# Kernel tuning notes

Measured on AMD Instinct MI355X. Metric: run time of the kernel, lower is better.

The kernel has to match this reference:

```python
import jax, jax.numpy as jnp
import numpy as np

N, D, H, L, E, OUT, G = 2048, 128, 8, 8, 65536, 64, 16
HD = D // H            # head_dim = 16
SCALE = HD ** -0.5
EPS = 1e-5             # BatchNorm1d eps


def _batchnorm(x, gamma, beta):
    # training-mode BatchNorm1d: biased batch stats over the node axis
    m = jnp.mean(x, axis=0)
    v = jnp.var(x, axis=0)
    return gamma * (x - m) * jax.lax.rsqrt(v + EPS) + beta


def _forward(X, pos_enc, proj_W, proj_b, pe_W, pe_b,
             Wq, bq, Wk, bk, Wv, bv, Wo, bo,
             g1, beta1, W1, b1, W2, b2, g2, beta2,
             mlp_W1, mlp_b1, mlp_W2, mlp_b2,
             edge_index, graph_ids, num_graphs):
    n = X.shape[0]
    # dense adjacency; sparse_coo_tensor sums duplicate edges -> scatter-add
    A = jnp.zeros((n, n), jnp.float32).at[edge_index[0], edge_index[1]].add(1.0)
    h = X @ proj_W + proj_b + pos_enc @ pe_W + pe_b          # [N, D]
    for l in range(L):
        h1 = h
        # NOTE: faithful to torch: [N,D] row-major reshaped to [H,N,HD]
        q = (h @ Wq[l] + bq[l]).reshape(H, n, HD) * SCALE
        k = (h @ Wk[l] + bk[l]).reshape(H, n, HD)
        v = (h @ Wv[l] + bv[l]).reshape(H, n, HD)
        t = jnp.einsum('hnd,hmd->hnm', q, k)                 # [H,N,N]
        attn = jax.nn.softmax(t * A, axis=2)                 # multiply-mask, softmax over all N
        o = jnp.einsum('hnm,hmd->hnd', attn, v).reshape(n, D)
        h = _batchnorm(o @ Wo[l] + bo[l] + h1, g1[l], beta1[l])
        h2 = h
        h = jax.nn.relu(h @ W1[l] + b1[l]) @ W2[l] + b2[l]
        h = _batchnorm(h2 + h, g2[l], beta2[l])
    # SumNode: per-graph node sum
    pooled = jax.ops.segment_sum(h, graph_ids, num_segments=num_graphs)  # [G, D]
    return jax.nn.relu(pooled @ mlp_W1 + mlp_b1) @ mlp_W2 + mlp_b2       # [G, OUT]


def setup_inputs() -> dict:
    key = jax.random.key(0)
    ks = jax.random.split(key, 32)
    f = jnp.float32
    s = D ** -0.5
    inp = {
        'X': jax.random.normal(ks[0], (N, 4), f),
        'pos_enc': jax.random.normal(ks[1], (N, 2), f),
        'edge_index': jax.random.randint(ks[2], (2, E), 0, N),
        'graph_ids': jnp.sort(jax.random.randint(ks[3], (N,), 0, G)).astype(jnp.int32),
        'num_graphs': G,
        'proj_W': jax.random.normal(ks[4], (4, D), f) * 0.5,
        'proj_b': jnp.zeros((D,), f),
        'pe_W': jax.random.normal(ks[5], (2, D), f) * 0.5,
        'pe_b': jnp.zeros((D,), f),
        'Wq': jax.random.normal(ks[6], (L, D, D), f) * s,
        'bq': jnp.zeros((L, D), f),
        'Wk': jax.random.normal(ks[7], (L, D, D), f) * s,
        'bk': jnp.zeros((L, D), f),
        'Wv': jax.random.normal(ks[8], (L, D, D), f) * s,
        'bv': jnp.zeros((L, D), f),
        'Wo': jax.random.normal(ks[9], (L, D, D), f) * s,
        'bo': jnp.zeros((L, D), f),
        'g1': jnp.ones((L, D), f),
        'beta1': jnp.zeros((L, D), f),
        'W1': jax.random.normal(ks[10], (L, D, 2 * D), f) * s,
        'b1': jnp.zeros((L, 2 * D), f),
        'W2': jax.random.normal(ks[11], (L, 2 * D, D), f) * (2 * D) ** -0.5,
        'b2': jnp.zeros((L, D), f),
        'g2': jnp.ones((L, D), f),
        'beta2': jnp.zeros((L, D), f),
        'mlp_W1': jax.random.normal(ks[12], (D, D), f) * s,
        'mlp_b1': jnp.zeros((D,), f),
        'mlp_W2': jax.random.normal(ks[13], (D, OUT), f) * s,
        'mlp_b2': jnp.zeros((OUT,), f),
    }
    return inp


def reference(X, pos_enc, edge_index, graph_ids, num_graphs,
              proj_W, proj_b, pe_W, pe_b,
              Wq, bq, Wk, bk, Wv, bv, Wo, bo,
              g1, beta1, W1, b1, W2, b2, g2, beta2,
              mlp_W1, mlp_b1, mlp_W2, mlp_b2):
    return _forward(X, pos_enc, proj_W, proj_b, pe_W, pe_b,
                    Wq, bq, Wk, bk, Wv, bv, Wo, bo,
                    g1, beta1, W1, b1, W2, b2, g2, beta2,
                    mlp_W1, mlp_b1, mlp_W2, mlp_b2,
                    edge_index, graph_ids, num_graphs)
```

## Files before the change

kernel.cpp:

```cpp
#include <hip/hip_runtime.h>
#include <hip/hip_bf16.h>

#define NN 2048
#define DD 128
#define HH 8
#define HDIM 16
#define LL 8
#define GG 16
#define BNEPS 1e-5f

typedef unsigned int u32;
typedef unsigned long long u64;
typedef __attribute__((ext_vector_type(8))) short bf16x8;
typedef __attribute__((ext_vector_type(8))) unsigned short us8;
typedef __attribute__((ext_vector_type(4))) float f32x4;

__device__ __forceinline__ unsigned short f2bf(float f) {
    union { float f; u32 u; } v; v.f = f;
    u32 u = v.u;
    u32 r = (u + 0x7fffu + ((u >> 16) & 1u)) >> 16;
    return (unsigned short)r;
}

__global__ __launch_bounds__(256) void zero_k(uint4* __restrict__ p) {
    p[blockIdx.x * 256 + threadIdx.x] = make_uint4(0u, 0u, 0u, 0u);
}

__global__ __launch_bounds__(256) void scatter_k(const int* __restrict__ ei, u32* __restrict__ A, int E) {
    int e = blockIdx.x * 256 + threadIdx.x;
    if (e < E) {
        int s = ei[e];
        int d = ei[E + e];
        atomicAdd(&A[s * NN + d], 1u);
    }
}

__global__ __launch_bounds__(256) void count_k(const u32* __restrict__ A, u32* __restrict__ deg) {
    int r = blockIdx.x, t = threadIdx.x;
    __shared__ u32 sb[256];
    u32 c = 0;
    for (int j = t; j < NN; j += 256) c += (A[r * NN + j] != 0u) ? 1u : 0u;
    sb[t] = c; __syncthreads();
    for (int off = 128; off; off >>= 1) { if (t < off) sb[t] += sb[t + off]; __syncthreads(); }
    if (t == 0) deg[r] = sb[0];
}

__global__ __launch_bounds__(256) void scan_k(const u32* __restrict__ deg, u32* __restrict__ rowptr) {
    __shared__ u32 part[256];
    int t = threadIdx.x;
    u32 loc[8]; u32 s = 0;
#pragma unroll
    for (int i = 0; i < 8; i++) { loc[i] = deg[t * 8 + i]; s += loc[i]; }
    part[t] = s; __syncthreads();
    for (int off = 1; off < 256; off <<= 1) {
        u32 vprev = (t >= off) ? part[t - off] : 0u;
        __syncthreads();
        part[t] += vprev;
        __syncthreads();
    }
    u32 run = (t == 0) ? 0u : part[t - 1];
    if (t == 0) rowptr[0] = 0u;
#pragma unroll
    for (int i = 0; i < 8; i++) { run += loc[i]; rowptr[t * 8 + i + 1] = run; }
}

__global__ __launch_bounds__(256) void emit_k(const u32* __restrict__ A, const u32* __restrict__ rowptr,
                                              u32* __restrict__ colidx, u32* __restrict__ cntv) {
    int r = blockIdx.x, tid = threadIdx.x;
    int lane = tid & 63, wid = tid >> 6;
    __shared__ u32 wsum[4];
    u32 base = rowptr[r];
    u32 cb = 0;
    for (int c0 = 0; c0 < NN; c0 += 256) {
        int c = c0 + tid;
        u32 a = A[r * NN + c];
        bool p = (a != 0u);
        u64 bal = __ballot(p);
        u32 rankw = (u32)__popcll(bal & ((1ull << lane) - 1ull));
        if (lane == 0) wsum[wid] = (u32)__popcll(bal);
        __syncthreads();
        u32 woff = 0;
#pragma unroll
        for (int w2 = 0; w2 < 4; w2++) if (w2 < wid) woff += wsum[w2];
        u32 tot = wsum[0] + wsum[1] + wsum[2] + wsum[3];
        if (p) { u32 pos = base + cb + woff + rankw; colidx[pos] = (u32)c; cntv[pos] = a; }
        cb += tot;
        __syncthreads();
    }
}

__global__ __launch_bounds__(256) void wconv_k(const float* __restrict__ Wq, const float* __restrict__ Wk,
                                               const float* __restrict__ Wv, const float* __restrict__ Wo,
                                               const float* __restrict__ W1, const float* __restrict__ W2,
                                               us8* __restrict__ Wf) {
    int tid = blockIdx.x * 256 + threadIdx.x;
    int layer = tid >> 14;
    int r = tid & 16383;
// ... 21 lines not shown
    int col = nt * 16 + (lane & 15);
    int k0 = kt * 32 + (lane >> 4) * 8;
    us8 o;
#pragma unroll
    for (int j = 0; j < 8; j++) o[j] = f2bf(src[(k0 + j) * ld + col]);
    Wf[tid] = o;
}

__global__ __launch_bounds__(256) void h0_k(const float* __restrict__ X, const float* __restrict__ pe,
                                            const float* __restrict__ pW, const float* __restrict__ pb,
                                            const float* __restrict__ peW, const float* __restrict__ peb,
                                            float* __restrict__ h) {
    int idx = blockIdx.x * 256 + threadIdx.x;
    int r = idx >> 7, d = idx & 127;
    float acc = pb[d] + peb[d];
    acc += X[r * 4 + 0] * pW[0 * DD + d];
    acc += X[r * 4 + 1] * pW[1 * DD + d];
    acc += X[r * 4 + 2] * pW[2 * DD + d];
    acc += X[r * 4 + 3] * pW[3 * DD + d];
    acc += pe[r * 2 + 0] * peW[0 * DD + d];
    acc += pe[r * 2 + 1] * peW[1 * DD + d];
    h[idx] = acc;
}

__device__ __forceinline__ void finalize_stats2(const float* __restrict__ ps, const float* __restrict__ pss,
                                                const float* __restrict__ gamma, const float* __restrict__ beta,
                                                float* aS, float* cS, float* sred, int tidx) {
    if (ps) {
        int d = tidx & 127, half = tidx >> 7;
        float s = 0.f, s2 = 0.f;
        const float* p0 = ps + half * 64 * 128 + d;
        const float* p1 = pss + half * 64 * 128 + d;
#pragma unroll 8
        for (int i = 0; i < 64; i++) { s += p0[i * 128]; s2 += p1[i * 128]; }
        sred[tidx] = s;
        sred[256 + tidx] = s2;
        __syncthreads();
        if (tidx < 128) {
            float st = sred[tidx] + sred[tidx + 128];
            float s2t = sred[256 + tidx] + sred[256 + tidx + 128];
            float mean = st * (1.0f / NN);
            float var = s2t * (1.0f / NN) - mean * mean;
            float rstd = rsqrtf(var + BNEPS);
            float a = gamma[tidx] * rstd;
            aS[tidx] = a;
            cS[tidx] = beta[tidx] - mean * a;
        }
    } else if (tidx < 128) {
        aS[tidx] = 1.f;
        cS[tidx] = 0.f;
    }
}

__global__ __launch_bounds__(256) void qkv_k(const float* __restrict__ t,
                                             const float* __restrict__ ps, const float* __restrict__ pss,
                                             const float* __restrict__ gamma, const float* __restrict__ beta,
                                             const bf16x8* __restrict__ Wfl,
                                             const float* __restrict__ bq, const float* __restrict__ bk,
                                             const float* __restrict__ bv,
                                             float* __restrict__ q, float* __restrict__ k, float* __restrict__ v,
                                             float* __restrict__ psv) {
    __shared__ float aS[128], cS[128], sred[512];
    int tidx = threadIdx.x;
    finalize_stats2(ps, pss, gamma, beta, aS, cS, sred, tidx);
    __syncthreads();
    int strip = blockIdx.x;
    int m0 = strip * 16;
    int lane = tidx & 63, wv = tidx >> 6;
    int arow = m0 + (lane & 15);
    int k0b = (lane >> 4) * 8;
    bf16x8 af[4];
#pragma unroll
    for (int kt = 0; kt < 4; kt++) {
        int k0 = kt * 32 + k0b;
        const float* tp = t + arow * DD + k0;
        float4 v0 = *(const float4*)(tp);
        float4 v1 = *(const float4*)(tp + 4);
        float vals[8] = {v0.x, v0.y, v0.z, v0.w, v1.x, v1.y, v1.z, v1.w};
        bf16x8 f;
#pragma unroll
        for (int j = 0; j < 8; j++) f[j] = (short)f2bf(vals[j] * aS[k0 + j] + cS[k0 + j]);
        af[kt] = f;
    }
#pragma unroll
    for (int ti = 0; ti < 6; ti++) {
        int tile = wv * 6 + ti;
        int mat = tile >> 3, nt = tile & 7;
        const bf16x8* wb = Wfl + mat * 2048;
        f32x4 acc = {0.f, 0.f, 0.f, 0.f};
#pragma unroll
        for (int kt = 0; kt < 4; kt++)
            acc = __builtin_amdgcn_mfma_f32_16x16x32_bf16(af[kt], wb[(kt * 8 + nt) * 64 + lane], acc, 0, 0, 0);
        const float* bias = (mat == 0) ? bq : ((mat == 1) ? bk : bv);
        float* outp = (mat == 0) ? q : ((mat == 1) ? k : v);
        float scale = (mat == 0) ? 0.25f : 1.0f;
        int col = nt * 16 + (lane & 15);
        int r0 = m0 + (lane >> 4) * 4;
        float bb = bias[col];
        float vals[4];
#pragma unroll
        for (int j = 0; j < 4; j++) {
            vals[j] = (acc[j] + bb) * scale;
            outp[(r0 + j) * DD + col] = vals[j];
        }
        if (mat == 2) {
            float cs = vals[0] + vals[1] + vals[2] + vals[3];
            cs += __shfl_xor(cs, 16);
            cs += __shfl_xor(cs, 32);
            if (lane < 16) psv[strip * 128 + col] = cs;
        }
    }
}

__global__ __launch_bounds__(256) void attn2_k(const float* __restrict__ q, const float* __restrict__ kb,
                                               const float* __restrict__ vb, const u32* __restrict__ rowptr,
                                               const u32* __restrict__ colidx, const u32* __restrict__ cntv,
                                               const float* __restrict__ psv, unsigned short* __restrict__ obb) {
    int tid = threadIdx.x;
    int bid = blockIdx.x;
    int hh = bid >> 7;
    __shared__ float vred[16][17];
    __shared__ float vsS[16];
    {
        int d = tid & 15, part = tid >> 4;
        int strip = hh * 16 + part;
        float s = 0.f;
#pragma unroll
        for (int i = 0; i < 8; i++) s += psv[strip * 128 + i * 16 + d];
        vred[d][part] = s;
    }
    __syncthreads();
    if (tid < 16) {
        float s = 0.f;
#pragma unroll
        for (int i = 0; i < 16; i++) s += vred[tid][i];
        vsS[tid] = s;
    }
    __syncthreads();

    int lane = tid & 15;
    int gidx = bid * 16 + (tid >> 4);
    int nn = gidx & (NN - 1);
    const float* qr = q + hh * (NN * HDIM) + nn * HDIM;
    float qv[16];
    *(float4*)&qv[0]  = *(const float4*)(qr + 0);
    *(float4*)&qv[4]  = *(const float4*)(qr + 4);
    *(float4*)&qv[8]  = *(const float4*)(qr + 8);
    *(float4*)&qv[12] = *(const float4*)(qr + 12);
    int rs = (int)rowptr[nn], re = (int)rowptr[nn + 1];
    int deg = re - rs;

    float s[8];
    int mc[8];
    float lm = -1e30f;
#pragma unroll
    for (int ch = 0; ch < 8; ch++) {
        s[ch] = -1e30f; mc[ch] = 0;
        if (ch * 16 < deg) {
            int e = rs + ch * 16 + lane;
            if (e < re) {
                mc[ch] = (int)colidx[e];
                float c = (float)cntv[e];
                const float* kr = kb + hh * (NN * HDIM) + mc[ch] * HDIM;
                float kv[16];
                *(float4*)&kv[0]  = *(const float4*)(kr + 0);
                *(float4*)&kv[4]  = *(const float4*)(kr + 4);
                *(float4*)&kv[8]  = *(const float4*)(kr + 8);
                *(float4*)&kv[12] = *(const float4*)(kr + 12);
                float d = 0.f;
#pragma unroll
                for (int i = 0; i < 16; i++) d += qv[i] * kv[i];
                s[ch] = c * d;
            }
            lm = fmaxf(lm, s[ch]);
        }
// ... 14 lines not shown
    for (int off = 1; off < 16; off <<= 1) lm = fmaxf(lm, __shfl_xor(lm, off));
    float rowmax = fmaxf(lm, 0.f);
    float em = __expf(-rowmax);

    float z = 0.f;
    float acc[16];
#pragma unroll
    for (int i = 0; i < 16; i++) acc[i] = 0.f;
#pragma unroll
    for (int ch = 0; ch < 8; ch++) {
        if (ch * 16 < deg) {
            int e = rs + ch * 16 + lane;
            if (e < re) {
                float w = __expf(s[ch] - rowmax);
                z += w;
                float coef = w - em;
                const float* vr = vb + hh * (NN * HDIM) + mc[ch] * HDIM;
                float vv[16];
                *(float4*)&vv[0]  = *(const float4*)(vr + 0);
                *(float4*)&vv[4]  = *(const float4*)(vr + 4);
                *(float4*)&vv[8]  = *(const float4*)(vr + 8);
                *(float4*)&vv[12] = *(const float4*)(vr + 12);
#pragma unroll
                for (int i = 0; i < 16; i++) acc[i] += coef * vv[i];
            }
        }
    }
    for (int base = rs + 128; base < re; base += 16) {
        int e = base + lane;
        if (e < re) {
            int m2 = (int)colidx[e];
            float c = (float)cntv[e];
            const float* kr = kb + hh * (NN * HDIM) + m2 * HDIM;
            float d = 0.f;
#pragma unroll
            for (int i = 0; i < 16; i++) d += qv[i] * kr[i];
            float w = __expf(c * d - rowmax);
            z += w;
            float coef = w - em;
            const float* vr = vb + hh * (NN * HDIM) + m2 * HDIM;
#pragma unroll
            for (int i = 0; i < 16; i++) acc[i] += coef * vr[i];
        }
    }
#pragma unroll
    for (int off = 1; off < 16; off <<= 1) {
        z += __shfl_xor(z, off);
#pragma unroll
        for (int i = 0; i < 16; i++) acc[i] += __shfl_xor(acc[i], off);
    }
    if (lane == 0) {
        float Z = z + (float)(NN - deg) * em;
        float inv = 1.f / Z;
        unsigned short* orow = obb + hh * (NN * HDIM) + nn * HDIM;
        us8 lo, hi;
#pragma unroll
        for (int i = 0; i < 8; i++) {
            lo[i] = f2bf((acc[i] + em * vsS[i]) * inv);
            hi[i] = f2bf((acc[i + 8] + em * vsS[i + 8]) * inv);
        }
        *(us8*)(orow + 0) = lo;
        *(us8*)(orow + 8) = hi;
    }
}

__global__ __launch_bounds__(256) void gemmO_k(const unsigned short* __restrict__ obb,
                                               const bf16x8* __restrict__ Wfo,
                                               const float* __restrict__ bo,
                                               const float* __restrict__ tprev,
                                               const float* __restrict__ ps, const float* __restrict__ pss,
                                               const float* __restrict__ gamma, const float* __restrict__ beta,
                                               float* __restrict__ t1,
                                               float* __restrict__ ps1, float* __restrict__ pss1) {
    __shared__ float aS[128], cS[128], sred[512];
    int tidx = threadIdx.x;
    finalize_stats2(ps, pss, gamma, beta, aS, cS, sred, tidx);
    __syncthreads();
    int strip = blockIdx.x;
    int m0 = strip * 16;
    int lane = tidx & 63, wv = tidx >> 6;
    int arow = m0 + (lane & 15);
    int k0b = (lane >> 4) * 8;
    bf16x8 af[4];
#pragma unroll
    for (int kt = 0; kt < 4; kt++)
        af[kt] = *(const bf16x8*)(obb + arow * DD + kt * 32 + k0b);
#pragma unroll
    for (int ti = 0; ti < 2; ti++) {
        int nt = wv * 2 + ti;
        f32x4 acc = {0.f, 0.f, 0.f, 0.f};
#pragma unroll
        for (int kt = 0; kt < 4; kt++)
            acc = __builtin_amdgcn_mfma_f32_16x16x32_bf16(af[kt], Wfo[(kt * 8 + nt) * 64 + lane], acc, 0, 0, 0);
        int col = nt * 16 + (lane & 15);
        int r0 = m0 + (lane >> 4) * 4;
        float bb = bo[col];
        float a = aS[col], c = cS[col];
        float sum = 0.f, sumsq = 0.f;
#pragma unroll
        for (int j = 0; j < 4; j++) {
            float res = tprev[(r0 + j) * DD + col] * a + c;
            float v0 = acc[j] + bb + res;
            t1[(r0 + j) * DD + col] = v0;
            sum += v0; sumsq += v0 * v0;
        }
        sum += __shfl_xor(sum, 16);  sum += __shfl_xor(sum, 32);
        sumsq += __shfl_xor(sumsq, 16); sumsq += __shfl_xor(sumsq, 32);
        if (lane < 16) { ps1[strip * 128 + col] = sum; pss1[strip * 128 + col] = sumsq; }
    }
}

__global__ __launch_bounds__(256) void mlp_k(const float* __restrict__ t1,
                                             const float* __restrict__ ps1, const float* __restrict__ pss1,
                                             const float* __restrict__ g1, const float* __restrict__ be1,
                                             const bf16x8* __restrict__ Wf1, const float* __restrict__ b1,
                                             const bf16x8* __restrict__ Wf2, const float* __restrict__ b2,
                                             float* __restrict__ t2,
                                             float* __restrict__ ps2, float* __restrict__ pss2) {
    __shared__ float aS[128], cS[128], sred[512];
    __shared__ unsigned short midL[16][264];
    int tidx = threadIdx.x;
    finalize_stats2(ps1, pss1, g1, be1, aS, cS, sred, tidx);
    __syncthreads();
    int strip = blockIdx.x;
    int m0 = strip * 16;
    int lane = tidx & 63, wv = tidx >> 6;
    int lrow = lane & 15;
    int arow = m0 + lrow;
    int k0b = (lane >> 4) * 8;
    bf16x8 af[4];
#pragma unroll
    for (int kt = 0; kt < 4; kt++) {
        int k0 = kt * 32 + k0b;
        const float* tp = t1 + arow * DD + k0;
        float4 v0 = *(const float4*)(tp);
        float4 v1 = *(const float4*)(tp + 4);
        float vals[8] = {v0.x, v0.y, v0.z, v0.w, v1.x, v1.y, v1.z, v1.w};
        bf16x8 f;
#pragma unroll
        for (int j = 0; j < 8; j++) f[j] = (short)f2bf(vals[j] * aS[k0 + j] + cS[k0 + j]);
        af[kt] = f;
    }
#pragma unroll
    for (int ti = 0; ti < 4; ti++) {
        int nt = wv * 4 + ti;
        f32x4 acc = {0.f, 0.f, 0.f, 0.f};
#pragma unroll
        for (int kt = 0; kt < 4; kt++)
            acc = __builtin_amdgcn_mfma_f32_16x16x32_bf16(af[kt], Wf1[(kt * 16 + nt) * 64 + lane], acc, 0, 0, 0);
        int col = nt * 16 + (lane & 15);
        int r0l = (lane >> 4) * 4;
        float bb = b1[col];
#pragma unroll
        for (int j = 0; j < 4; j++)
            midL[r0l + j][col] = f2bf(fmaxf(acc[j] + bb, 0.f));
    }
    __syncthreads();
    bf16x8 af2[8];
#pragma unroll
    for (int kt = 0; kt < 8; kt++)
        af2[kt] = *(const bf16x8*)(&midL[lrow][kt * 32 + k0b]);
#pragma unroll
    for (int ti = 0; ti < 2; ti++) {
        int nt = wv * 2 + ti;
        f32x4 acc = {0.f, 0.f, 0.f, 0.f};
#pragma unroll
        for (int kt = 0; kt < 8; kt++)
            acc = __builtin_amdgcn_mfma_f32_16x16x32_bf16(af2[kt], Wf2[(kt * 8 + nt) * 64 + lane], acc, 0, 0, 0);
        int col = nt * 16 + (lane & 15);
        int r0 = m0 + (lane >> 4) * 4;
        float bb = b2[col];
        float a = aS[col], c = cS[col];
        float sum = 0.f, sumsq = 0.f;
#pragma unroll
        for (int j = 0; j < 4; j++) {
            float res = t1[(r0 + j) * DD + col] * a + c;
            float v0 = acc[j] + bb + res;
            t2[(r0 + j) * DD + col] = v0;
            sum += v0; sumsq += v0 * v0;
        }
        sum += __shfl_xor(sum, 16);  sum += __shfl_xor(sum, 32);
        sumsq += __shfl_xor(sumsq, 16); sumsq += __shfl_xor(sumsq, 32);
        if (lane < 16) { ps2[strip * 128 + col] = sum; pss2[strip * 128 + col] = sumsq; }
    }
}

__global__ __launch_bounds__(128) void poolpart_k(const float* __restrict__ t, const float* __restrict__ ps,
                                                  const float* __restrict__ pss, const float* __restrict__ gamma,
                                                  const float* __restrict__ beta, const int* __restrict__ gid,
                                                  float* __restrict__ poolp) {
    int g = blockIdx.x;
    int ch = blockIdx.y;
    int d = threadIdx.x;
    float s = 0.f, s2 = 0.f;
#pragma unroll 8
    for (int i = 0; i < 128; i++) { s += ps[i * 128 + d]; s2 += pss[i * 128 + d]; }
    float mean = s * (1.0f / NN);
    float var = s2 * (1.0f / NN) - mean * mean;
    float rstd = rsqrtf(var + BNEPS);
    float a = gamma[d] * rstd;
    float c = beta[d] - mean * a;
    int lo = 0, hi = NN;
    while (lo < hi) { int mid = (lo + hi) >> 1; if (gid[mid] < g) lo = mid + 1; else hi = mid; }
    int start = lo;
    lo = start; hi = NN;
    while (lo < hi) { int mid = (lo + hi) >> 1; if (gid[mid] <= g) lo = mid + 1; else hi = mid; }
    int end = lo;
    float acc = 0.f;
    for (int r = start + ch; r < end; r += 8) acc += t[r * DD + d] * a + c;
    poolp[(g * 8 + ch) * DD + d] = acc;
}

__global__ __launch_bounds__(256) void head_k(const float* __restrict__ poolp, const float* __restrict__ W1,
                                              const float* __restrict__ b1, const float* __restrict__ W2,
                                              const float* __restrict__ b2, float* __restrict__ out) {
    int g = blockIdx.x;
    __shared__ float p[128], midv[128];
    if (threadIdx.x < 128) {
        float s = 0.f;
#pragma unroll
        for (int c = 0; c < 8; c++) s += poolp[(g * 8 + c) * DD + threadIdx.x];
        p[threadIdx.x] = s;
    }
    __syncthreads();
    if (threadIdx.x < 128) {
        int d = threadIdx.x;
        float acc = b1[d];
        for (int k2 = 0; k2 < 128; k2++) acc += p[k2] * W1[k2 * 128 + d];
        midv[d] = fmaxf(acc, 0.f);
    }
    __syncthreads();
    if (threadIdx.x < 64) {
        int j = threadIdx.x;
        float acc = b2[j];
        for (int k2 = 0; k2 < 128; k2++) acc += midv[k2] * W2[k2 * 64 + j];
        out[g * 64 + j] = acc;
    }
}

extern "C" void kernel_launch(void* const* d_in, const int* in_sizes, int n_in,
                              void* d_out, int out_size, void* d_ws, size_t ws_size,
                              hipStream_t stream) {
    (void)n_in; (void)out_size; (void)ws_size;
    const float* X      = (const float*)d_in[0];
    const float* pos    = (const float*)d_in[1];
    const int*   ei     = (const int*)d_in[2];
    const int*   gid    = (const int*)d_in[3];
    const float* proj_W = (const float*)d_in[5];
    const float* proj_b = (const float*)d_in[6];
    const float* pe_W   = (const float*)d_in[7];
    const float* pe_b   = (const float*)d_in[8];
    const float* Wq     = (const float*)d_in[9];
    const float* bq     = (const float*)d_in[10];
    const float* Wk     = (const float*)d_in[11];
    const float* bk     = (const float*)d_in[12];
    const float* Wv     = (const float*)d_in[13];
    const float* bv     = (const float*)d_in[14];
    const float* Wo     = (const float*)d_in[15];
    const float* bo     = (const float*)d_in[16];
    const float* g1     = (const float*)d_in[17];
    const float* beta1  = (const float*)d_in[18];
    const float* W1     = (const float*)d_in[19];
    const float* b1     = (const float*)d_in[20];
    const float* W2     = (const float*)d_in[21];
    const float* b2     = (const float*)d_in[22];
    const float* g2     = (const float*)d_in[23];
    const float* beta2  = (const float*)d_in[24];
    const float* mW1    = (const float*)d_in[25];
    const float* mb1    = (const float*)d_in[26];
    const float* mW2    = (const float*)d_in[27];
    const float* mb2    = (const float*)d_in[28];
    float* out = (float*)d_out;

    int E = in_sizes[2] / 2;

    char* w = (char*)d_ws;
    u32*   Adense = (u32*)(w + 0);
    u32*   deg    = (u32*)(w + 16777216);
    u32*   rowptr = (u32*)(w + 16785408);
    u32*   colidx = (u32*)(w + 16793856);
    u32*   cntv   = (u32*)(w + 17056000);
    float* tA     = (float*)(w + 17318144);
    float* tB     = (float*)(w + 18366720);
    float* qb     = (float*)(w + 19415296);
    float* kb     = (float*)(w + 20463872);
    float* vb     = (float*)(w + 21512448);
    unsigned short* obb = (unsigned short*)(w + 22561024);
    float* psA    = (float*)(w + 23085312);
    float* pssA   = (float*)(w + 23150848);
    float* psB    = (float*)(w + 23216384);
    float* pssB   = (float*)(w + 23281920);
    float* psv    = (float*)(w + 23347456);
    bf16x8* Wf    = (bf16x8*)(w + 23421184);
    float* poolp  = (float*)(w + 25518336);

    zero_k<<<4096, 256, 0, stream>>>((uint4*)Adense);
    scatter_k<<<(E + 255) / 256, 256, 0, stream>>>(ei, Adense, E);
    count_k<<<NN, 256, 0, stream>>>(Adense, deg);
    scan_k<<<1, 256, 0, stream>>>(deg, rowptr);
    emit_k<<<NN, 256, 0, stream>>>(Adense, rowptr, colidx, cntv);

    wconv_k<<<512, 256, 0, stream>>>(Wq, Wk, Wv, Wo, W1, W2, (us8*)Wf);

    h0_k<<<NN * DD / 256, 256, 0, stream>>>(X, pos, proj_W, proj_b, pe_W, pe_b, tA);

    for (int l = 0; l < LL; l++) {
        const bf16x8* Wfl = Wf + l * 16384;
        const float* psIn  = (l == 0) ? nullptr : psA;
        const float* pssIn = (l == 0) ? nullptr : pssA;
        const float* gIn   = (l == 0) ? nullptr : (g2 + (l - 1) * DD);
        const float* bIn   = (l == 0) ? nullptr : (beta2 + (l - 1) * DD);

        qkv_k<<<128, 256, 0, stream>>>(tA, psIn, pssIn, gIn, bIn, Wfl,
                                       bq + l * DD, bk + l * DD, bv + l * DD, qb, kb, vb, psv);
        attn2_k<<<HH * NN / 16, 256, 0, stream>>>(qb, kb, vb, rowptr, colidx, cntv, psv, obb);
        gemmO_k<<<128, 256, 0, stream>>>(obb, Wfl + 6144, bo + l * DD, tA, psIn, pssIn, gIn, bIn,
                                         tB, psB, pssB);
        mlp_k<<<128, 256, 0, stream>>>(tB, psB, pssB, g1 + l * DD, beta1 + l * DD,
                                       Wfl + 8192, b1 + l * 2 * DD, Wfl + 12288, b2 + l * DD,
                                       tA, psA, pssA);
    }

    poolpart_k<<<dim3(GG, 8), 128, 0, stream>>>(tA, psA, pssA, g2 + 7 * DD, beta2 + 7 * DD, gid, poolp);
    head_k<<<GG, 256, 0, stream>>>(poolp, mW1, mb1, mW2, mb2, out);
}
```

Baseline: 336.7 us.

## Fuse per-layer kernels into one persistent cooperative kernel with grid syncs

After: 431.8 us. 1.28x slower.

```diff
diff --git a/kernel.cpp b/kernel.cpp
--- a/kernel.cpp
+++ b/kernel.cpp
@@ -1,4 +1,5 @@
 #include <hip/hip_runtime.h>
+#include <hip/hip_cooperative_groups.h>
 #include <hip/hip_bf16.h>
 
 #define NN 2048
@@ -8,6 +9,8 @@
 #define LL 8
 #define GG 16
 #define BNEPS 1e-5f
+
+namespace cg = cooperative_groups;
 
 typedef unsigned int u32;
 typedef unsigned long long u64;
@@ -170,19 +173,17 @@
     }
 }
 
-__global__ __launch_bounds__(256) void qkv_k(const float* __restrict__ t,
-                                             const float* __restrict__ ps, const float* __restrict__ pss,
-                                             const float* __restrict__ gamma, const float* __restrict__ beta,
-                                             const bf16x8* __restrict__ Wfl,
-                                             const float* __restrict__ bq, const float* __restrict__ bk,
-                                             const float* __restrict__ bv,
-                                             float* __restrict__ q, float* __restrict__ k, float* __restrict__ v,
-                                             float* __restrict__ psv) {
+__device__ void qkv_phase(const float* __restrict__ t,
+                          const float* __restrict__ ps, const float* __restrict__ pss,
+                          const float* __restrict__ gamma, const float* __restrict__ beta,
+                          const bf16x8* __restrict__ Wfl,
+                          const float* __restrict__ bq, const float* __restrict__ bk,
+                          const float* __restrict__ bv,
+                          float* __restrict__ q, float* __restrict__ k, float* __restrict__ v,
+                          float* __restrict__ psv, int strip, int tidx) {
     __shared__ float aS[128], cS[128], sred[512];
-    int tidx = threadIdx.x;
     finalize_stats2(ps, pss, gamma, beta, aS, cS, sred, tidx);
     __syncthreads();
-    int strip = blockIdx.x;
     int m0 = strip * 16;
     int lane = tidx & 63, wv = tidx >> 6;
     int arow = m0 + (lane & 15);
@@ -230,12 +231,11 @@
     }
 }
 
-__global__ __launch_bounds__(256) void attn2_k(const float* __restrict__ q, const float* __restrict__ kb,
-                                               const float* __restrict__ vb, const u32* __restrict__ rowptr,
-                                               const u32* __restrict__ colidx, const u32* __restrict__ cntv,
-                                               const float* __restrict__ psv, unsigned short* __restrict__ obb) {
-    int tid = threadIdx.x;
-    int bid = blockIdx.x;
+__device__ void attn_phase(const float* __restrict__ q, const float* __restrict__ kb,
+                           const float* __restrict__ vb, const u32* __restrict__ rowptr,
+                           const u32* __restrict__ colidx, const u32* __restrict__ cntv,
+                           const float* __restrict__ psv, unsigned short* __restrict__ obb,
+                           int bid, int tid) {
     int hh = bid >> 7;
     __shared__ float vred[16][17];
     __shared__ float vsS[16];
@@ -371,19 +371,17 @@
     }
 }
 
-__global__ __launch_bounds__(256) void gemmO_k(const unsigned short* __restrict__ obb,
-                                               const bf16x8* __restrict__ Wfo,
-                                               const float* __restrict__ bo,
-                                               const float* __restrict__ tprev,
-                                               const float* __restrict__ ps, const float* __restrict__ pss,
-                                               const float* __restrict__ gamma, const float* __restrict__ beta,
-                                               float* __restrict__ t1,
-                                               float* __restrict__ ps1, float* __restrict__ pss1) {
+__device__ void gemmO_phase(const unsigned short* __restrict__ obb,
+                            const bf16x8* __restrict__ Wfo,
+                            const float* __restrict__ bo,
+                            const float* __restrict__ tprev,
+                            const float* __restrict__ ps, const float* __restrict__ pss,
+                            const float* __restrict__ gamma, const float* __restrict__ beta,
+                            float* __restrict__ t1,
+                            float* __restrict__ ps1, float* __restrict__ pss1, int strip, int tidx) {
     __shared__ float aS[128], cS[128], sred[512];
-    int tidx = threadIdx.x;
     finalize_stats2(ps, pss, gamma, beta, aS, cS, sred, tidx);
     __syncthreads();
-    int strip = blockIdx.x;
     int m0 = strip * 16;
     int lane = tidx & 63, wv = tidx >> 6;
     int arow = m0 + (lane & 15);
@@ -417,19 +415,17 @@
     }
 }
 
-__global__ __launch_bounds__(256) void mlp_k(const float* __restrict__ t1,
-                                             const float* __restrict__ ps1, const float* __restrict__ pss1,
-                                             const float* __restrict__ g1, const float* __restrict__ be1,
-                                             const bf16x8* __restrict__ Wf1, const float* __restrict__ b1,
-                                             const bf16x8* __restrict__ Wf2, const float* __restrict__ b2,
-                                             float* __restrict__ t2,
-                                             float* __restrict__ ps2, float* __restrict__ pss2) {
+__device__ void mlp_phase(const float* __restrict__ t1,
+                          const float* __restrict__ ps1, const float* __restrict__ pss1,
+                          const float* __restrict__ g1, const float* __restrict__ be1,
+                          const bf16x8* __restrict__ Wf1, const float* __restrict__ b1,
+                          const bf16x8* __restrict__ Wf2, const float* __restrict__ b2,
+                          float* __restrict__ t2,
+                          float* __restrict__ ps2, float* __restrict__ pss2, int strip, int tidx) {
     __shared__ float aS[128], cS[128], sred[512];
     __shared__ unsigned short midL[16][264];
-    int tidx = threadIdx.x;
     finalize_stats2(ps1, pss1, g1, be1, aS, cS, sred, tidx);
     __syncthreads();
-    int strip = blockIdx.x;
     int m0 = strip * 16;
     int lane = tidx & 63, wv = tidx >> 6;
     int lrow = lane & 15;
@@ -492,13 +488,14 @@
     }
 }
 
-__global__ __launch_bounds__(128) void poolpart_k(const float* __restrict__ t, const float* __restrict__ ps,
-                                                  const float* __restrict__ pss, const float* __restrict__ gamma,
-                                                  const float* __restrict__ beta, const int* __restrict__ gid,
-                                                  float* __restrict__ poolp) {
-    int g = blockIdx.x;
-    int ch = blockIdx.y;
-    int d = threadIdx.x;
+__device__ void poolpart_phase(const float* __restrict__ t, const float* __restrict__ ps,
+                               const float* __restrict__ pss, const float* __restrict__ gamma,
+                               const float* __restrict__ beta, const int* __restrict__ gid,
+                               float* __restrict__ poolp, int bid, int tidx) {
+    if (tidx >= 128) return;
+    int g = bid >> 3;
+    int ch = bid & 7;
+    int d = tidx;
     float s = 0.f, s2 = 0.f;
 #pragma unroll 8
     for (int i = 0; i < 128; i++) { s += ps[i * 128 + d]; s2 += pss[i * 128 + d]; }
@@ -518,31 +515,109 @@
     poolp[(g * 8 + ch) * DD + d] = acc;
 }
 
-__global__ __launch_bounds__(256) void head_k(const float* __restrict__ poolp, const float* __restrict__ W1,
-                                              const float* __restrict__ b1, const float* __restrict__ W2,
-                                              const float* __restrict__ b2, float* __restrict__ out) {
-    int g = blockIdx.x;
+__device__ void head_phase(const float* __restrict__ poolp, const float* __restrict__ W1,
+                           const float* __restrict__ b1, const float* __restrict__ W2,
+                           const float* __restrict__ b2, float* __restrict__ out, int g, int tidx) {
     __shared__ float p[128], midv[128];
-    if (threadIdx.x < 128) {
+    if (tidx < 128) {
         float s = 0.f;
 #pragma unroll
-        for (int c = 0; c < 8; c++) s += poolp[(g * 8 + c) * DD + threadIdx.x];
-        p[threadIdx.x] = s;
+        for (int c = 0; c < 8; c++) s += poolp[(g * 8 + c) * DD + tidx];
+        p[tidx] = s;
     }
     __syncthreads();
-    if (threadIdx.x < 128) {
-        int d = threadIdx.x;
+    if (tidx < 128) {
+        int d = tidx;
         float acc = b1[d];
         for (int k2 = 0; k2 < 128; k2++) acc += p[k2] * W1[k2 * 128 + d];
         midv[d] = fmaxf(acc, 0.f);
     }
     __syncthreads();
-    if (threadIdx.x < 64) {
-        int j = threadIdx.x;
+    if (tidx < 64) {
+        int j = tidx;
         float acc = b2[j];
         for (int k2 = 0; k2 < 128; k2++) acc += midv[k2] * W2[k2 * 64 + j];
         out[g * 64 + j] = acc;
     }
+}
+
+struct LayerParams {
+    const u32 *rowptr, *colidx, *cntv;
+    const bf16x8* Wf;
+    const float *bq, *bk, *bv, *bo, *g1, *be1, *b1, *b2, *g2, *be2;
+    const float *mW1, *mb1, *mW2, *mb2;
+    const int* gid;
+    float *tA, *tB, *qb, *kb, *vb;
+    unsigned short* obb;
+    float *psA, *pssA, *psB, *pssB, *psv, *poolp;
+    float* out;
+};
+
+__global__ __launch_bounds__(256, 4) void layers_k(LayerParams P) {
+    cg::grid_group grid = cg::this_grid();
+    int bid = blockIdx.x, tidx = threadIdx.x;
+#pragma clang loop unroll(disable)
+    for (int l = 0; l < LL; l++) {
+        const bf16x8* Wfl = P.Wf + l * 16384;
+        const float* psIn  = (l == 0) ? nullptr : P.psA;
+        const float* pssIn = (l == 0) ? nullptr : P.pssA;
+        const float* gIn   = (l == 0) ? nullptr : (P.g2 + (l - 1) * DD);
+        const float* bIn   = (l == 0) ? nullptr : (P.be2 + (l - 1) * DD);
+        if (bid < 128)
+            qkv_phase(P.tA, psIn, pssIn, gIn, bIn, Wfl, P.bq + l * DD, P.bk + l * DD, P.bv + l * DD,
+                      P.qb, P.kb, P.vb, P.psv, bid, tidx);
+        grid.sync();
+        attn_phase(P.qb, P.kb, P.vb, P.rowptr, P.colidx, P.cntv, P.psv, P.obb, bid, tidx);
+        grid.sync();
+        if (bid < 128)
+            gemmO_phase(P.obb, Wfl + 6144, P.bo + l * DD, P.tA, psIn, pssIn, gIn, bIn,
+                        P.tB, P.psB, P.pssB, bid, tidx);
+        grid.sync();
+        if (bid < 128)
+            mlp_phase(P.tB, P.psB, P.pssB, P.g1 + l * DD, P.be1 + l * DD,
+                      Wfl + 8192, P.b1 + l * 2 * DD, Wfl + 12288, P.b2 + l * DD,
+                      P.tA, P.psA, P.pssA, bid, tidx);
+        grid.sync();
+    }
+    if (bid < 128)
+        poolpart_phase(P.tA, P.psA, P.pssA, P.g2 + 7 * DD, P.be2 + 7 * DD, P.gid, P.poolp, bid, tidx);
+    grid.sync();
+    if (bid < 16)
+        head_phase(P.poolp, P.mW1, P.mb1, P.mW2, P.mb2, P.out, bid, tidx);
+}
+
+__global__ __launch_bounds__(256) void qkv_k(const float* t, const float* ps, const float* pss,
+                                             const float* gamma, const float* beta, const bf16x8* Wfl,
+                                             const float* bq, const float* bk, const float* bv,
+                                             float* q, float* k, float* v, float* psv) {
+    qkv_phase(t, ps, pss, gamma, beta, Wfl, bq, bk, bv, q, k, v, psv, blockIdx.x, threadIdx.x);
+}
+__global__ __launch_bounds__(256) void attn2_k(const float* q, const float* kb, const float* vb,
+                                               const u32* rowptr, const u32* colidx, const u32* cntv,
+                                               const float* psv, unsigned short* obb) {
+    attn_phase(q, kb, vb, rowptr, colidx, cntv, psv, obb, blockIdx.x, threadIdx.x);
+}
+__global__ __launch_bounds__(256) void gemmO_k(const unsigned short* obb, const bf16x8* Wfo, const float* bo,
+                                               const float* tprev, const float* ps, const float* pss,
+                                               const float* gamma, const float* beta,
+                                               float* t1, float* ps1, float* pss1) {
+    gemmO_phase(obb, Wfo, bo, tprev, ps, pss, gamma, beta, t1, ps1, pss1, blockIdx.x, threadIdx.x);
+}
+__global__ __launch_bounds__(256) void mlp_k(const float* t1, const float* ps1, const float* pss1,
+                                             const float* g1, const float* be1,
+                                             const bf16x8* Wf1, const float* b1,
+                                             const bf16x8* Wf2, const float* b2,
+                                             float* t2, float* ps2, float* pss2) {
+    mlp_phase(t1, ps1, pss1, g1, be1, Wf1, b1, Wf2, b2, t2, ps2, pss2, blockIdx.x, threadIdx.x);
+}
+__global__ __launch_bounds__(256) void poolpart_k(const float* t, const float* ps, const float* pss,
+                                                  const float* gamma, const float* beta, const int* gid,
+                                                  float* poolp) {
+    poolpart_phase(t, ps, pss, gamma, beta, gid, poolp, blockIdx.x, threadIdx.x);
+}
+__global__ __launch_bounds__(256) void head_k(const float* poolp, const float* W1, const float* b1,
+                                              const float* W2, const float* b2, float* out) {
+    head_phase(poolp, W1, b1, W2, b2, out, blockIdx.x, threadIdx.x);
 }
 
 extern "C" void kernel_launch(void* const* d_in, const int* in_sizes, int n_in,
@@ -611,23 +686,46 @@
 
     h0_k<<<NN * DD / 256, 256, 0, stream>>>(X, pos, proj_W, proj_b, pe_W, pe_b, tA);
 
-    for (int l = 0; l < LL; l++) {
-        const bf16x8* Wfl = Wf + l * 16384;
-        const float* psIn  = (l == 0) ? nullptr : psA;
-        const float* pssIn = (l == 0) ? nullptr : pssA;
-        const float* gIn   = (l == 0) ? nullptr : (g2 + (l - 1) * DD);
-        const float* bIn   = (l == 0) ? nullptr : (beta2 + (l - 1) * DD);
-
-        qkv_k<<<128, 256, 0, stream>>>(tA, psIn, pssIn, gIn, bIn, Wfl,
-                                       bq + l * DD, bk + l * DD, bv + l * DD, qb, kb, vb, psv);
-        attn2_k<<<HH * NN / 16, 256, 0, stream>>>(qb, kb, vb, rowptr, colidx, cntv, psv, obb);
-        gemmO_k<<<128, 256, 0, stream>>>(obb, Wfl + 6144, bo + l * DD, tA, psIn, pssIn, gIn, bIn,
-                                         tB, psB, pssB);
-        mlp_k<<<128, 256, 0, stream>>>(tB, psB, pssB, g1 + l * DD, beta1 + l * DD,
-                                       Wfl + 8192, b1 + l * 2 * DD, Wfl + 12288, b2 + l * DD,
-                                       tA, psA, pssA);
-    }
-
-    poolpart_k<<<dim3(GG, 8), 128, 0, stream>>>(tA, psA, pssA, g2 + 7 * DD, beta2 + 7 * DD, gid, poolp);
-    head_k<<<GG, 256, 0, stream>>>(poolp, mW1, mb1, mW2, mb2, out);
-}
+    LayerParams hp;
+    hp.rowptr = rowptr; hp.colidx = colidx; hp.cntv = cntv;
+    hp.Wf = Wf;
+    hp.bq = bq; hp.bk = bk; hp.bv = bv; hp.bo = bo;
+    hp.g1 = g1; hp.be1 = beta1; hp.b1 = b1; hp.b2 = b2; hp.g2 = g2; hp.be2 = beta2;
+    hp.mW1 = mW1; hp.mb1 = mb1; hp.mW2 = mW2; hp.mb2 = mb2;
+    hp.gid = gid;
+    hp.tA = tA; hp.tB = tB; hp.qb = qb; hp.kb = kb; hp.vb = vb;
+    hp.obb = obb;
+    hp.psA = psA; hp.pssA = pssA; hp.psB = psB; hp.pssB = pssB; hp.psv = psv; hp.poolp = poolp;
+    hp.out = out;
+
+    bool coop_ok = false;
+    int nb = 0;
+    if (hipOccupancyMaxActiveBlocksPerMultiprocessor(&nb, (const void*)layers_k, 256, 0) == hipSuccess) {
+        if (nb >= 4) coop_ok = true;
+    }
+    hipError_t ce = hipErrorUnknown;
+    if (coop_ok) {
+        void* kargs[] = { (void*)&hp };
+        ce = hipLaunchCooperativeKernel((const void*)layers_k, dim3(1024), dim3(256), kargs, 0, stream);
+    }
+    if (ce != hipSuccess) {
+        (void)hipGetLastError();
+        for (int l = 0; l < LL; l++) {
+            const bf16x8* Wfl = Wf + l * 16384;
+            const float* psIn  = (l == 0) ? nullptr : psA;
+            const float* pssIn = (l == 0) ? nullptr : pssA;
+            const float* gIn   = (l == 0) ? nullptr : (g2 + (l - 1) * DD);
+            const float* bIn   = (l == 0) ? nullptr : (beta2 + (l - 1) * DD);
+            qkv_k<<<128, 256, 0, stream>>>(tA, psIn, pssIn, gIn, bIn, Wfl,
+                                           bq + l * DD, bk + l * DD, bv + l * DD, qb, kb, vb, psv);
+            attn2_k<<<HH * NN / 16, 256, 0, stream>>>(qb, kb, vb, rowptr, colidx, cntv, psv, obb);
+            gemmO_k<<<128, 256, 0, stream>>>(obb, Wfl + 6144, bo + l * DD, tA, psIn, pssIn, gIn, bIn,
+                                             tB, psB, pssB);
+            mlp_k<<<128, 256, 0, stream>>>(tB, psB, pssB, g1 + l * DD, beta1 + l * DD,
+                                           Wfl + 8192, b1 + l * 2 * DD, Wfl + 12288, b2 + l * DD,
+                                           tA, psA, pssA);
+        }
+        poolpart_k<<<128, 256, 0, stream>>>(tA, psA, pssA, g2 + 7 * DD, beta2 + 7 * DD, gid, poolp);
+        head_k<<<GG, 256, 0, stream>>>(poolp, mW1, mb1, mW2, mb2, out);
+    }
+}
```

## Fuse output projection into attention kernel and merge pooling with head MLP

Applied to the files above, without the earlier changes.

After: 473.1 us. 1.41x slower.

```diff
diff --git a/kernel.cpp b/kernel.cpp
--- a/kernel.cpp
+++ b/kernel.cpp
@@ -170,6 +170,30 @@
     }
 }
 
+__device__ __forceinline__ void finalize_stats_1024(const float* __restrict__ ps, const float* __restrict__ pss,
+                                                    const float* __restrict__ gamma, const float* __restrict__ beta,
+                                                    float* aS, float* cS, float* sred, int tidx) {
+    int d = tidx & 127, half = tidx >> 7;
+    float s = 0.f, s2 = 0.f;
+    const float* p0 = ps + half * 512 * 128 + d;
+    const float* p1 = pss + half * 512 * 128 + d;
+#pragma unroll 8
+    for (int i = 0; i < 512; i++) { s += p0[i * 128]; s2 += p1[i * 128]; }
+    sred[tidx] = s;
+    sred[256 + tidx] = s2;
+    __syncthreads();
+    if (tidx < 128) {
+        float st = sred[tidx] + sred[tidx + 128];
+        float s2t = sred[256 + tidx] + sred[256 + tidx + 128];
+        float mean = st * (1.0f / NN);
+        float var = s2t * (1.0f / NN) - mean * mean;
+        float rstd = rsqrtf(var + BNEPS);
+        float a = gamma[tidx] * rstd;
+        aS[tidx] = a;
+        cS[tidx] = beta[tidx] - mean * a;
+    }
+}
+
 __global__ __launch_bounds__(256) void qkv_k(const float* __restrict__ t,
                                              const float* __restrict__ ps, const float* __restrict__ pss,
                                              const float* __restrict__ gamma, const float* __restrict__ beta,
@@ -177,7 +201,7 @@
                                              const float* __restrict__ bq, const float* __restrict__ bk,
                                              const float* __restrict__ bv,
                                              float* __restrict__ q, float* __restrict__ k, float* __restrict__ v,
-                                             float* __restrict__ psv) {
+                                             float* __restrict__ psv, float* __restrict__ tnorm) {
     __shared__ float aS[128], cS[128], sred[512];
     int tidx = threadIdx.x;
     finalize_stats2(ps, pss, gamma, beta, aS, cS, sred, tidx);
@@ -195,9 +219,17 @@
         float4 v0 = *(const float4*)(tp);
         float4 v1 = *(const float4*)(tp + 4);
         float vals[8] = {v0.x, v0.y, v0.z, v0.w, v1.x, v1.y, v1.z, v1.w};
+        float vn[8];
         bf16x8 f;
 #pragma unroll
-        for (int j = 0; j < 8; j++) f[j] = (short)f2bf(vals[j] * aS[k0 + j] + cS[k0 + j]);
+        for (int j = 0; j < 8; j++) {
+            vn[j] = vals[j] * aS[k0 + j] + cS[k0 + j];
+            f[j] = (short)f2bf(vn[j]);
+        }
+        if (wv == 0) {
+            *(float4*)(tnorm + arow * DD + k0)     = make_float4(vn[0], vn[1], vn[2], vn[3]);
+            *(float4*)(tnorm + arow * DD + k0 + 4) = make_float4(vn[4], vn[5], vn[6], vn[7]);
+        }
         af[kt] = f;
     }
 #pragma unroll
@@ -233,12 +265,17 @@
 __global__ __launch_bounds__(256) void attn2_k(const float* __restrict__ q, const float* __restrict__ kb,
                                                const float* __restrict__ vb, const u32* __restrict__ rowptr,
                                                const u32* __restrict__ colidx, const u32* __restrict__ cntv,
-                                               const float* __restrict__ psv, unsigned short* __restrict__ obb) {
+                                               const float* __restrict__ psv,
+                                               const bf16x8* __restrict__ Wfo, const float* __restrict__ bo,
+                                               const float* __restrict__ tnorm,
+                                               float* __restrict__ t1,
+                                               float* __restrict__ psB, float* __restrict__ pssB) {
     int tid = threadIdx.x;
     int bid = blockIdx.x;
     int hh = bid >> 7;
     __shared__ float vred[16][17];
     __shared__ float vsS[16];
+    __shared__ unsigned short oL[16][16];
     {
         int d = tid & 15, part = tid >> 4;
         int strip = hh * 16 + part;
@@ -359,61 +396,45 @@
     if (lane == 0) {
         float Z = z + (float)(NN - deg) * em;
         float inv = 1.f / Z;
-        unsigned short* orow = obb + hh * (NN * HDIM) + nn * HDIM;
-        us8 lo, hi;
-#pragma unroll
-        for (int i = 0; i < 8; i++) {
-            lo[i] = f2bf((acc[i] + em * vsS[i]) * inv);
-            hi[i] = f2bf((acc[i + 8] + em * vsS[i + 8]) * inv);
-        }
-        *(us8*)(orow + 0) = lo;
-        *(us8*)(orow + 8) = hi;
-    }
-}
-
-__global__ __launch_bounds__(256) void gemmO_k(const unsigned short* __restrict__ obb,
-                                               const bf16x8* __restrict__ Wfo,
-                                               const float* __restrict__ bo,
-                                               const float* __restrict__ tprev,
-                                               const float* __restrict__ ps, const float* __restrict__ pss,
-                                               const float* __restrict__ gamma, const float* __restrict__ beta,
-                                               float* __restrict__ t1,
-                                               float* __restrict__ ps1, float* __restrict__ pss1) {
-    __shared__ float aS[128], cS[128], sred[512];
-    int tidx = threadIdx.x;
-    finalize_stats2(ps, pss, gamma, beta, aS, cS, sred, tidx);
-    __syncthreads();
-    int strip = blockIdx.x;
-    int m0 = strip * 16;
-    int lane = tidx & 63, wv = tidx >> 6;
-    int arow = m0 + (lane & 15);
-    int k0b = (lane >> 4) * 8;
+        int grp = tid >> 4;
+#pragma unroll
+        for (int i = 0; i < 16; i++) oL[grp][i] = f2bf((acc[i] + em * vsS[i]) * inv);
+    }
+    __syncthreads();
+
+    int l64 = tid & 63, w = tid >> 6;
+    int row = l64 & 15, kq = l64 >> 4;
     bf16x8 af[4];
-#pragma unroll
-    for (int kt = 0; kt < 4; kt++)
-        af[kt] = *(const bf16x8*)(obb + arow * DD + kt * 32 + k0b);
+    if (row < 2) {
+#pragma unroll
+        for (int kt = 0; kt < 4; kt++)
+            af[kt] = *(const bf16x8*)&oL[row * 8 + kt * 2 + (kq >> 1)][(kq & 1) * 8];
+    } else {
+        bf16x8 zf = {0, 0, 0, 0, 0, 0, 0, 0};
+#pragma unroll
+        for (int kt = 0; kt < 4; kt++) af[kt] = zf;
+    }
 #pragma unroll
     for (int ti = 0; ti < 2; ti++) {
-        int nt = wv * 2 + ti;
-        f32x4 acc = {0.f, 0.f, 0.f, 0.f};
+        int nt = w * 2 + ti;
+        f32x4 oacc = {0.f, 0.f, 0.f, 0.f};
 #pragma unroll
         for (int kt = 0; kt < 4; kt++)
-            acc = __builtin_amdgcn_mfma_f32_16x16x32_bf16(af[kt], Wfo[(kt * 8 + nt) * 64 + lane], acc, 0, 0, 0);
-        int col = nt * 16 + (lane & 15);
-        int r0 = m0 + (lane >> 4) * 4;
-        float bb = bo[col];
-        float a = aS[col], c = cS[col];
-        float sum = 0.f, sumsq = 0.f;
-#pragma unroll
-        for (int j = 0; j < 4; j++) {
-            float res = tprev[(r0 + j) * DD + col] * a + c;
-            float v0 = acc[j] + bb + res;
-            t1[(r0 + j) * DD + col] = v0;
-            sum += v0; sumsq += v0 * v0;
-        }
-        sum += __shfl_xor(sum, 16);  sum += __shfl_xor(sum, 32);
-        sumsq += __shfl_xor(sumsq, 16); sumsq += __shfl_xor(sumsq, 32);
-        if (lane < 16) { ps1[strip * 128 + col] = sum; pss1[strip * 128 + col] = sumsq; }
+            oacc = __builtin_amdgcn_mfma_f32_16x16x32_bf16(af[kt], Wfo[(kt * 8 + nt) * 64 + l64], oacc, 0, 0, 0);
+        if (kq == 0) {
+            int col = nt * 16 + row;
+            float bb = bo[col];
+            float sum = 0.f, sumsq = 0.f;
+#pragma unroll
+            for (int j = 0; j < 2; j++) {
+                int r = 2 * bid + j;
+                float v0 = oacc[j] + bb + tnorm[r * DD + col];
+                t1[r * DD + col] = v0;
+                sum += v0; sumsq += v0 * v0;
+            }
+            psB[bid * 128 + col] = sum;
+            pssB[bid * 128 + col] = sumsq;
+        }
     }
 }
 
@@ -427,7 +448,7 @@
     __shared__ float aS[128], cS[128], sred[512];
     __shared__ unsigned short midL[16][264];
     int tidx = threadIdx.x;
-    finalize_stats2(ps1, pss1, g1, be1, aS, cS, sred, tidx);
+    finalize_stats_1024(ps1, pss1, g1, be1, aS, cS, sred, tidx);
     __syncthreads();
     int strip = blockIdx.x;
     int m0 = strip * 16;
@@ -492,56 +513,41 @@
     }
 }
 
-__global__ __launch_bounds__(128) void poolpart_k(const float* __restrict__ t, const float* __restrict__ ps,
-                                                  const float* __restrict__ pss, const float* __restrict__ gamma,
-                                                  const float* __restrict__ beta, const int* __restrict__ gid,
-                                                  float* __restrict__ poolp) {
-    int g = blockIdx.x;
-    int ch = blockIdx.y;
-    int d = threadIdx.x;
-    float s = 0.f, s2 = 0.f;
-#pragma unroll 8
-    for (int i = 0; i < 128; i++) { s += ps[i * 128 + d]; s2 += pss[i * 128 + d]; }
-    float mean = s * (1.0f / NN);
-    float var = s2 * (1.0f / NN) - mean * mean;
-    float rstd = rsqrtf(var + BNEPS);
-    float a = gamma[d] * rstd;
-    float c = beta[d] - mean * a;
+__global__ __launch_bounds__(256) void pool_head_k(const float* __restrict__ t, const float* __restrict__ ps,
+                                                   const float* __restrict__ pss, const float* __restrict__ gamma,
+                                                   const float* __restrict__ beta, const int* __restrict__ gid,
+                                                   const float* __restrict__ W1, const float* __restrict__ b1,
+                                                   const float* __restrict__ W2, const float* __restrict__ b2,
+                                                   float* __restrict__ out) {
+    __shared__ float aS[128], cS[128], sred[512];
+    __shared__ float psum[2][128];
+    __shared__ float p[128], midv[128];
+    int tidx = threadIdx.x, g = blockIdx.x;
+    finalize_stats2(ps, pss, gamma, beta, aS, cS, sred, tidx);
+    __syncthreads();
     int lo = 0, hi = NN;
     while (lo < hi) { int mid = (lo + hi) >> 1; if (gid[mid] < g) lo = mid + 1; else hi = mid; }
     int start = lo;
     lo = start; hi = NN;
     while (lo < hi) { int mid = (lo + hi) >> 1; if (gid[mid] <= g) lo = mid + 1; else hi = mid; }
     int end = lo;
+    int d = tidx & 127, half = tidx >> 7;
     float acc = 0.f;
-    for (int r = start + ch; r < end; r += 8) acc += t[r * DD + d] * a + c;
-    poolp[(g * 8 + ch) * DD + d] = acc;
-}
-
-__global__ __launch_bounds__(256) void head_k(const float* __restrict__ poolp, const float* __restrict__ W1,
-                                              const float* __restrict__ b1, const float* __restrict__ W2,
-                                              const float* __restrict__ b2, float* __restrict__ out) {
-    int g = blockIdx.x;
-    __shared__ float p[128], midv[128];
-    if (threadIdx.x < 128) {
-        float s = 0.f;
-#pragma unroll
-        for (int c = 0; c < 8; c++) s += poolp[(g * 8 + c) * DD + threadIdx.x];
-        p[threadIdx.x] = s;
-    }
-    __syncthreads();
-    if (threadIdx.x < 128) {
-        int d = threadIdx.x;
-        float acc = b1[d];
-        for (int k2 = 0; k2 < 128; k2++) acc += p[k2] * W1[k2 * 128 + d];
-        midv[d] = fmaxf(acc, 0.f);
-    }
-    __syncthreads();
-    if (threadIdx.x < 64) {
-        int j = threadIdx.x;
-        float acc = b2[j];
-        for (int k2 = 0; k2 < 128; k2++) acc += midv[k2] * W2[k2 * 64 + j];
-        out[g * 64 + j] = acc;
+    for (int r = start + half; r < end; r += 2) acc += t[r * DD + d] * aS[d] + cS[d];
+    psum[half][d] = acc;
+    __syncthreads();
+    if (tidx < 128) p[tidx] = psum[0][tidx] + psum[1][tidx];
+    __syncthreads();
+    if (tidx < 128) {
+        float a = b1[tidx];
+        for (int k2 = 0; k2 < 128; k2++) a += p[k2] * W1[k2 * 128 + tidx];
+        midv[tidx] = fmaxf(a, 0.f);
+    }
+    __syncthreads();
+    if (tidx < 64) {
+        float a = b2[tidx];
+        for (int k2 = 0; k2 < 128; k2++) a += midv[k2] * W2[k2 * 64 + tidx];
+        out[g * 64 + tidx] = a;
     }
 }
 
@@ -592,14 +598,13 @@
     float* qb     = (float*)(w + 19415296);
     float* kb     = (float*)(w + 20463872);
     float* vb     = (float*)(w + 21512448);
-    unsigned short* obb = (unsigned short*)(w + 22561024);
-    float* psA    = (float*)(w + 23085312);
-    float* pssA   = (float*)(w + 23150848);
-    float* psB    = (float*)(w + 23216384);
-    float* pssB   = (float*)(w + 23281920);
-    float* psv    = (float*)(w + 23347456);
-    bf16x8* Wf    = (bf16x8*)(w + 23421184);
-    float* poolp  = (float*)(w + 25518336);
+    float* tnorm  = (float*)(w + 22561024);
+    float* psA    = (float*)(w + 23609600);
+    float* pssA   = (float*)(w + 23675136);
+    float* psv    = (float*)(w + 23740672);
+    float* psB    = (float*)(w + 23806208);
+    float* pssB   = (float*)(w + 24330496);
+    bf16x8* Wf    = (bf16x8*)(w + 24854784);
 
     zero_k<<<4096, 256, 0, stream>>>((uint4*)Adense);
     scatter_k<<<(E + 255) / 256, 256, 0, stream>>>(ei, Adense, E);
@@ -619,15 +624,14 @@
         const float* bIn   = (l == 0) ? nullptr : (beta2 + (l - 1) * DD);
 
         qkv_k<<<128, 256, 0, stream>>>(tA, psIn, pssIn, gIn, bIn, Wfl,
-                                       bq + l * DD, bk + l * DD, bv + l * DD, qb, kb, vb, psv);
-        attn2_k<<<HH * NN / 16, 256, 0, stream>>>(qb, kb, vb, rowptr, colidx, cntv, psv, obb);
-        gemmO_k<<<128, 256, 0, stream>>>(obb, Wfl + 6144, bo + l * DD, tA, psIn, pssIn, gIn, bIn,
-                                         tB, psB, pssB);
+                                       bq + l * DD, bk + l * DD, bv + l * DD, qb, kb, vb, psv, tnorm);
+        attn2_k<<<HH * NN / 16, 256, 0, stream>>>(qb, kb, vb, rowptr, colidx, cntv, psv,
+                                                  Wfl + 6144, bo + l * DD, tnorm, tB, psB, pssB);
         mlp_k<<<128, 256, 0, stream>>>(tB, psB, pssB, g1 + l * DD, beta1 + l * DD,
                                        Wfl + 8192, b1 + l * 2 * DD, Wfl + 12288, b2 + l * DD,
                                        tA, psA, pssA);
     }
 
-    poolpart_k<<<dim3(GG, 8), 128, 0, stream>>>(tA, psA, pssA, g2 + 7 * DD, beta2 + 7 * DD, gid, poolp);
-    head_k<<<GG, 256, 0, stream>>>(poolp, mW1, mb1, mW2, mb2, out);
-}
+    pool_head_k<<<GG, 256, 0, stream>>>(tA, psA, pssA, g2 + 7 * DD, beta2 + 7 * DD, gid,
+                                        mW1, mb1, mW2, mb2, out);
+}
```

## Count degrees during scatter and fuse pooling with head MLP

Applied to the files above, without the earlier changes.

New measurement: 347.2 us. 1.03x slower.

```diff
diff --git a/kernel.cpp b/kernel.cpp
--- a/kernel.cpp
+++ b/kernel.cpp
@@ -26,23 +26,15 @@
     p[blockIdx.x * 256 + threadIdx.x] = make_uint4(0u, 0u, 0u, 0u);
 }
 
-__global__ __launch_bounds__(256) void scatter_k(const int* __restrict__ ei, u32* __restrict__ A, int E) {
+__global__ __launch_bounds__(256) void scatter_k(const int* __restrict__ ei, u32* __restrict__ A,
+                                                 u32* __restrict__ deg, int E) {
     int e = blockIdx.x * 256 + threadIdx.x;
     if (e < E) {
         int s = ei[e];
         int d = ei[E + e];
-        atomicAdd(&A[s * NN + d], 1u);
-    }
-}
-
-__global__ __launch_bounds__(256) void count_k(const u32* __restrict__ A, u32* __restrict__ deg) {
-    int r = blockIdx.x, t = threadIdx.x;
-    __shared__ u32 sb[256];
-    u32 c = 0;
-    for (int j = t; j < NN; j += 256) c += (A[r * NN + j] != 0u) ? 1u : 0u;
-    sb[t] = c; __syncthreads();
-    for (int off = 128; off; off >>= 1) { if (t < off) sb[t] += sb[t + off]; __syncthreads(); }
-    if (t == 0) deg[r] = sb[0];
+        u32 old = atomicAdd(&A[s * NN + d], 1u);
+        if (old == 0u) atomicAdd(&deg[s], 1u);
+    }
 }
 
 __global__ __launch_bounds__(256) void scan_k(const u32* __restrict__ deg, u32* __restrict__ rowptr) {
@@ -492,56 +484,41 @@
     }
 }
 
-__global__ __launch_bounds__(128) void poolpart_k(const float* __restrict__ t, const float* __restrict__ ps,
-                                                  const float* __restrict__ pss, const float* __restrict__ gamma,
-                                                  const float* __restrict__ beta, const int* __restrict__ gid,
-                                                  float* __restrict__ poolp) {
-    int g = blockIdx.x;
-    int ch = blockIdx.y;
-    int d = threadIdx.x;
-    float s = 0.f, s2 = 0.f;
-#pragma unroll 8
-    for (int i = 0; i < 128; i++) { s += ps[i * 128 + d]; s2 += pss[i * 128 + d]; }
-    float mean = s * (1.0f / NN);
-    float var = s2 * (1.0f / NN) - mean * mean;
-    float rstd = rsqrtf(var + BNEPS);
-    float a = gamma[d] * rstd;
-    float c = beta[d] - mean * a;
+__global__ __launch_bounds__(256) void pool_head_k(const float* __restrict__ t, const float* __restrict__ ps,
+                                                   const float* __restrict__ pss, const float* __restrict__ gamma,
+                                                   const float* __restrict__ beta, const int* __restrict__ gid,
+                                                   const float* __restrict__ W1, const float* __restrict__ b1,
+                                                   const float* __restrict__ W2, const float* __restrict__ b2,
+                                                   float* __restrict__ out) {
+    __shared__ float aS[128], cS[128], sred[512];
+    __shared__ float psum[2][128];
+    __shared__ float p[128], midv[128];
+    int tidx = threadIdx.x, g = blockIdx.x;
+    finalize_stats2(ps, pss, gamma, beta, aS, cS, sred, tidx);
+    __syncthreads();
     int lo = 0, hi = NN;
     while (lo < hi) { int mid = (lo + hi) >> 1; if (gid[mid] < g) lo = mid + 1; else hi = mid; }
     int start = lo;
     lo = start; hi = NN;
     while (lo < hi) { int mid = (lo + hi) >> 1; if (gid[mid] <= g) lo = mid + 1; else hi = mid; }
     int end = lo;
+    int d = tidx & 127, half = tidx >> 7;
     float acc = 0.f;
-    for (int r = start + ch; r < end; r += 8) acc += t[r * DD + d] * a + c;
-    poolp[(g * 8 + ch) * DD + d] = acc;
-}
-
-__global__ __launch_bounds__(256) void head_k(const float* __restrict__ poolp, const float* __restrict__ W1,
-                                              const float* __restrict__ b1, const float* __restrict__ W2,
-                                              const float* __restrict__ b2, float* __restrict__ out) {
-    int g = blockIdx.x;
-    __shared__ float p[128], midv[128];
-    if (threadIdx.x < 128) {
-        float s = 0.f;
-#pragma unroll
-        for (int c = 0; c < 8; c++) s += poolp[(g * 8 + c) * DD + threadIdx.x];
-        p[threadIdx.x] = s;
-    }
-    __syncthreads();
-    if (threadIdx.x < 128) {
-        int d = threadIdx.x;
-        float acc = b1[d];
-        for (int k2 = 0; k2 < 128; k2++) acc += p[k2] * W1[k2 * 128 + d];
-        midv[d] = fmaxf(acc, 0.f);
-    }
-    __syncthreads();
-    if (threadIdx.x < 64) {
-        int j = threadIdx.x;
-        float acc = b2[j];
-        for (int k2 = 0; k2 < 128; k2++) acc += midv[k2] * W2[k2 * 64 + j];
-        out[g * 64 + j] = acc;
+    for (int r = start + half; r < end; r += 2) acc += t[r * DD + d] * aS[d] + cS[d];
+    psum[half][d] = acc;
+    __syncthreads();
+    if (tidx < 128) p[tidx] = psum[0][tidx] + psum[1][tidx];
+    __syncthreads();
+    if (tidx < 128) {
+        float a = b1[tidx];
+        for (int k2 = 0; k2 < 128; k2++) a += p[k2] * W1[k2 * 128 + tidx];
+        midv[tidx] = fmaxf(a, 0.f);
+    }
+    __syncthreads();
+    if (tidx < 64) {
+        float a = b2[tidx];
+        for (int k2 = 0; k2 < 128; k2++) a += midv[k2] * W2[k2 * 64 + tidx];
+        out[g * 64 + tidx] = a;
     }
 }
 
@@ -599,11 +576,9 @@
     float* pssB   = (float*)(w + 23281920);
     float* psv    = (float*)(w + 23347456);
     bf16x8* Wf    = (bf16x8*)(w + 23421184);
-    float* poolp  = (float*)(w + 25518336);
-
-    zero_k<<<4096, 256, 0, stream>>>((uint4*)Adense);
-    scatter_k<<<(E + 255) / 256, 256, 0, stream>>>(ei, Adense, E);
-    count_k<<<NN, 256, 0, stream>>>(Adense, deg);
+
+    zero_k<<<4098, 256, 0, stream>>>((uint4*)Adense);
+    scatter_k<<<(E + 255) / 256, 256, 0, stream>>>(ei, Adense, deg, E);
     scan_k<<<1, 256, 0, stream>>>(deg, rowptr);
     emit_k<<<NN, 256, 0, stream>>>(Adense, rowptr, colidx, cntv);
 
@@ -628,6 +603,6 @@
                                        tA, psA, pssA);
     }
 
-    poolpart_k<<<dim3(GG, 8), 128, 0, stream>>>(tA, psA, pssA, g2 + 7 * DD, beta2 + 7 * DD, gid, poolp);
-    head_k<<<GG, 256, 0, stream>>>(poolp, mW1, mb1, mW2, mb2, out);
-}
+    pool_head_k<<<GG, 256, 0, stream>>>(tA, psA, pssA, g2 + 7 * DD, beta2 + 7 * DD, gid,
+                                        mW1, mb1, mW2, mb2, out);
+}
```
